# Kernel tuning notes

Measured on AMD Instinct MI355X. Metric: run time of the kernel, lower is better.

## Reference

```python
import jax, jax.numpy as jnp
import numpy as np

N, E, IN_DIM, OUT_DIM, H = 4096, 131072, 1024, 512, 4


def setup_inputs() -> dict:
    key = jax.random.key(0)
    k1, k2, k3, k4 = jax.random.split(key, 4)
    x = jax.random.normal(k1, (N, IN_DIM), dtype=jnp.float32)
    edge_index = jax.random.randint(k2, (2, E), 0, N, dtype=jnp.int64)
    # learned params, scaled like torch Linear init (~1/sqrt(fan_in))
    W = jax.random.normal(k3, (H, IN_DIM, OUT_DIM), dtype=jnp.float32) * 0.02
    a = jax.random.normal(k4, (H, 2 * OUT_DIM), dtype=jnp.float32) * 0.02
    return {"x": x, "edge_index": edge_index, "W": W, "a": a}


def reference(x, edge_index, W, a):
    row, col = edge_index[0], edge_index[1]
    n = x.shape[0]
    h = jnp.einsum('ni,hio->hno', x, W)                    # [H, N, out]
    # per-edge attention logits: a . [h[row] || h[col]]
    a_src, a_dst = a[:, :OUT_DIM], a[:, OUT_DIM:]
    e = (jnp.einsum('heo,ho->he', h[:, row], a_src)
         + jnp.einsum('heo,ho->he', h[:, col], a_dst))      # [H, E]
    e = jnp.where(e > 0, e, 0.2 * e)                        # LeakyReLU(0.2)
    # dense NxN attention matrix exactly as the original (zeros at non-edges
    # DO participate in the row softmax, matching the torch code)
    att = jnp.zeros((H, n, n), dtype=h.dtype).at[:, row, col].set(e)
    att = jax.nn.softmax(att, axis=-1)
    h_prime = jnp.einsum('hnm,hmo->hno', att, h)            # [H, N, out]
    return jnp.transpose(h_prime, (1, 0, 2)).reshape(n, H * OUT_DIM)
```

## Files before the change

### kernel.cpp

```cpp
#include <hip/hip_runtime.h>
#include <stdint.h>

#define NN 4096
#define EE 131072
#define IND 1024
#define OUTD 512
#define NH 4
#define NBKT 8
#define BKT_SHIFT 9

typedef __bf16 bf16x8 __attribute__((ext_vector_type(8)));
typedef float f32x4 __attribute__((ext_vector_type(4)));
typedef float f32x2 __attribute__((ext_vector_type(2)));

__device__ __forceinline__ unsigned short f2bf(float f) {
  unsigned u = __float_as_uint(f);
  u += 0x7FFFu + ((u >> 16) & 1u);
  return (unsigned short)(u >> 16);
}

__global__ void prep_kernel(const float* __restrict__ x, unsigned short* __restrict__ xb,
                            const float* __restrict__ W, unsigned short* __restrict__ Wt) {
  __shared__ float tile[32][33];
  const int bid = blockIdx.x, t = threadIdx.x;
  if (bid < 4096) {
    int i = bid * 256 + t;
    float4 v = ((const float4*)x)[i];
    ushort4 o;
    o.x = f2bf(v.x); o.y = f2bf(v.y); o.z = f2bf(v.z); o.w = f2bf(v.w);
    ((ushort4*)xb)[i] = o;
  } else {
    int b2 = bid - 4096;
    int i0 = (b2 & 31) * 32, o0 = ((b2 >> 5) & 15) * 32, h = b2 >> 9;
    int tx = t & 31, ty = t >> 5;
#pragma unroll
    for (int r = 0; r < 32; r += 8)
      tile[ty + r][tx] = W[((size_t)(h * IND + i0 + ty + r)) * OUTD + o0 + tx];
    __syncthreads();
#pragma unroll
    for (int r = 0; r < 32; r += 8)
      Wt[((size_t)(h * OUTD + o0 + ty + r)) * IND + i0 + tx] = f2bf(tile[tx][ty + r]);
  }
}

__device__ __forceinline__ void gload16(const unsigned short* g, unsigned short* l) {
  __builtin_amdgcn_global_load_lds((const __attribute__((address_space(1))) void*)g,
                                   (__attribute__((address_space(3))) void*)l, 16, 0, 0);
}

__global__ __launch_bounds__(256, 2) void gemm_kernel(
    const unsigned short* __restrict__ X, const unsigned short* __restrict__ Wt,
    const float* __restrict__ Av, unsigned char* __restrict__ Hb8,
    float* __restrict__ s4_src, float* __restrict__ s4_dst, float* __restrict__ Scol) {
  __shared__ __align__(16) unsigned short As[2][4096];
  __shared__ __align__(16) unsigned short Bs[2][4096];
  const int t = threadIdx.x, w = t >> 6, lane = t & 63;
  const int B = blockIdx.x;
  const int L = ((B & 7) << 6) | (B >> 3);
  const int bx = L & 3, hh = (L >> 2) & 3, by = L >> 4;

  const unsigned short* Ab0 = X + (size_t)(by * 128) * IND;
  const unsigned short* Bb0 = Wt + (size_t)(hh * OUTD + bx * 128) * IND;

  const int seg0 = w * 64 + lane, seg1 = (4 + w) * 64 + lane;
  const int r0 = seg0 >> 2, c0 = (seg0 & 3) ^ (r0 & 3);
  const int r1 = seg1 >> 2, c1 = (seg1 & 3) ^ (r1 & 3);

  const int wr = w >> 1, wc = w & 1, g = lane >> 4, rlo = lane & 15;
  int aoff[4], boff[4];
#pragma unroll
  for (int i = 0; i < 4; i++) {
    int ra = wr * 64 + i * 16 + rlo;
    aoff[i] = ra * 64 + ((g ^ (ra & 3)) << 4);
    int rb = wc * 64 + i * 16 + rlo;
    boff[i] = rb * 64 + ((g ^ (rb & 3)) << 4);
  }

  f32x4 zero = {0.f, 0.f, 0.f, 0.f};
  f32x4 acc[4][4];
#pragma unroll
  for (int i = 0; i < 4; i++)
#pragma unroll
    for (int j = 0; j < 4; j++) acc[i][j] = zero;

#define STAGE(buf, kt)                                                   \
  do {                                                                   \
    const unsigned short* ga = Ab0 + (kt) * 32;                          \
    const unsigned short* gb = Bb0 + (kt) * 32;                          \
    gload16(ga + r0 * IND + c0 * 8, &As[buf][w * 512]);                  \
    gload16(ga + r1 * IND + c1 * 8, &As[buf][(4 + w) * 512]);            \
    gload16(gb + r0 * IND + c0 * 8, &Bs[buf][w * 512]);                  \
    gload16(gb + r1 * IND + c1 * 8, &Bs[buf][(4 + w) * 512]);            \
  } while (0)

  STAGE(0, 0);
  __syncthreads();
  int cur = 0;
  for (int kt = 0; kt < 32; ++kt) {
    if (kt != 31) STAGE(cur ^ 1, kt + 1);
    const char* Abuf = (const char*)As[cur];
    const char* Bbuf = (const char*)Bs[cur];
    bf16x8 av[4], bv[4];
#pragma unroll
    for (int i = 0; i < 4; i++) {
      av[i] = *(const bf16x8*)(Abuf + aoff[i]);
      bv[i] = *(const bf16x8*)(Bbuf + boff[i]);
    }
#pragma unroll
    for (int i = 0; i < 4; i++)
#pragma unroll
      for (int j = 0; j < 4; j++)
        acc[i][j] = __builtin_amdgcn_mfma_f32_16x16x32_bf16(av[i], bv[j], acc[i][j], 0, 0, 0);
    __syncthreads();
    cur ^= 1;
  }
#undef STAGE

#pragma unroll
  for (int i = 0; i < 4; i++)
#pragma unroll
    for (int j = 0; j < 4; j++) {
      int mm0 = by * 128 + wr * 64 + i * 16 + g * 4;
      int nn = bx * 128 + wc * 64 + j * 16 + rlo;
#pragma unroll
      for (int q = 0; q < 4; q++) {
        int p = __builtin_amdgcn_cvt_pk_fp8_f32(acc[i][j][q], acc[i][j][q], 0, false);
        Hb8[((size_t)(mm0 + q) * NH + hh) * OUTD + nn] = (unsigned char)p;
      }
    }

  float as_[4], ad_[4];
#pragma unroll
  for (int j = 0; j < 4; j++) {
    int nn = bx * 128 + wc * 64 + j * 16 + rlo;
    as_[j] = Av[hh * 2 * OUTD + nn];
    ad_[j] = Av[hh * 2 * OUTD + OUTD + nn];
  }
#pragma unroll
  for (int i = 0; i < 4; i++)
#pragma unroll
    for (int q = 0; q < 4; q++) {
      float vs = 0.f, vd = 0.f;
#pragma unroll
      for (int j = 0; j < 4; j++) {
        float tv = acc[i][j][q];
        vs += tv * as_[j];
        vd += tv * ad_[j];
      }
#pragma unroll
      for (int m = 1; m < 16; m <<= 1) {
        vs += __shfl_xor(vs, m);
        vd += __shfl_xor(vd, m);
      }
      if (rlo == 0) {
        int r = by * 128 + wr * 64 + i * 16 + g * 4 + q;
        atomicAdd(&s4_src[r * NH + hh], vs);
        atomicAdd(&s4_dst[r * NH + hh], vd);
      }
    }

#pragma unroll
  for (int j = 0; j < 4; j++) {
    float cv = 0.f;
#pragma unroll
    for (int i = 0; i < 4; i++)
#pragma unroll
      for (int q = 0; q < 4; q++) cv += acc[i][j][q];
    cv += __shfl_xor(cv, 16);
    cv += __shfl_xor(cv, 32);
    if (g == 0) {
      int nn = bx * 128 + wc * 64 + j * 16 + rlo;
      atomicAdd(&Scol[hh * OUTD + nn], cv);
    }
  }
}

__global__ void edge_a_kernel(const int* __restrict__ ei, unsigned* __restrict__ bitmap,
                              int* __restrict__ counts2, unsigned char* __restrict__ flags) {
  int e = blockIdx.x * 256 + threadIdx.x;
  int row = ei[e], col = ei[EE + e];
  unsigned key = ((unsigned)row << 12) | (unsigned)col;
  unsigned bit = 1u << (key & 31);
  unsigned old = atomicOr(&bitmap[key >> 5], bit);
  if (old & bit) { flags[e] = 1; return; }
  flags[e] = 0;
  atomicAdd(&counts2[row * NBKT + (col >> BKT_SHIFT)], 1);
}

__global__ __launch_bounds__(1024) void scan_kernel(const int* __restrict__ c2,
                                                    int* __restrict__ off2,
                                                    int* __restrict__ cur2) {
  __shared__ int wtot[16];
  const int t = threadIdx.x, w = t >> 6, lane = t & 63;
  int loc[32];
  const int4* src = (const int4*)c2 + t * 8;
#pragma unroll
  for (int k = 0; k < 8; k++) {
    int4 v = src[k];
    loc[4 * k] = v.x; loc[4 * k + 1] = v.y; loc[4 * k + 2] = v.z; loc[4 * k + 3] = v.w;
  }
  int s = 0;
#pragma unroll
  for (int k = 0; k < 32; k++) s += loc[k];
  int inc = s;
#pragma unroll
  for (int d = 1; d < 64; d <<= 1) {
    int u = __shfl_up(inc, d);
    if (lane >= d) inc += u;
  }
  if (lane == 63) wtot[w] = inc;
  __syncthreads();
  int wpre = 0;
  for (int k = 0; k < 16; k++)
    if (k < w) wpre += wtot[k];
  int o = wpre + inc - s;
  if (t == 1023) off2[NN * NBKT] = o + s;
  int4* od = (int4*)off2 + t * 8;
  int4* cd = (int4*)cur2 + t * 8;
#pragma unroll
  for (int k = 0; k < 8; k++) {
    int4 ov;
    ov.x = o; o += loc[4 * k];
    ov.y = o; o += loc[4 * k + 1];
    ov.z = o; o += loc[4 * k + 2];
    ov.w = o; o += loc[4 * k + 3];
    od[k] = ov;
    cd[k] = ov;
  }
}

__global__ void edge_b_kernel(const int* __restrict__ ei, const unsigned char* __restrict__ flags,
                              const float* __restrict__ s4_src, const float* __restrict__ s4_dst,
                              int* __restrict__ cursor2, int* __restrict__ csr_col,
                              float* __restrict__ csr_g4) {
  int e = blockIdx.x * 256 + threadIdx.x;
  if (flags[e]) return;
  int row = ei[e], col = ei[EE + e];
  int pos = atomicAdd(&cursor2[row * NBKT + (col >> BKT_SHIFT)], 1);
  csr_col[pos] = col;
  float4 ss = *(const float4*)(s4_src + row * NH);
  float4 sd = *(const float4*)(s4_dst + col * NH);
  float4 gv;
  float e0 = ss.x + sd.x; e0 = e0 > 0.f ? e0 : 0.2f * e0; gv.x = expf(e0) - 1.0f;
  float e1 = ss.y + sd.y; e1 = e1 > 0.f ? e1 : 0.2f * e1; gv.y = expf(e1) - 1.0f;
  float e2 = ss.z + sd.z; e2 = e2 > 0.f ? e2 : 0.2f * e2; gv.z = expf(e2) - 1.0f;
  float e3 = ss.w + sd.w; e3 = e3 > 0.f ? e3 : 0.2f * e3; gv.w = expf(e3) - 1.0f;
  *(float4*)(csr_g4 + (size_t)pos * NH) = gv;
}

__global__ __launch_bounds__(256) void finalize_kernel(
    const unsigned char* __restrict__ Hb8,
    const float* __restrict__ S, const int* __restrict__ offsets2,
    const int* __restrict__ csr_col, const float* __restrict__ csr_g4,
    float* __restrict__ out) {
  __shared__ int cols_s[64];
  __shared__ float g_s[4][64];
  const int i = blockIdx.x, t = threadIdx.x;
  const int w = t >> 6, lane = t & 63;

  float acc[8];
  {
    const float4* Sv = (const float4*)(S + w * OUTD + lane * 8);
    float4 s0 = Sv[0], s1 = Sv[1];
    acc[0] = s0.x; acc[1] = s0.y; acc[2] = s0.z; acc[3] = s0.w;
    acc[4] = s1.x; acc[5] = s1.y; acc[6] = s1.z; acc[7] = s1.w;
  }
  float gsum = 0.f;

  const int start = offsets2[i * NBKT];
  const int cnt = offsets2[(i + 1) * NBKT] - start;
  for (int base = 0; base < cnt; base += 64) {
    int nload = min(64, cnt - base);
    __syncthreads();
    if (w == 0) cols_s[lane] = (lane < nload) ? csr_col[start + base + lane] : 0;
    {
      int el = t >> 2;
      float gvv = (el < nload) ? csr_g4[(size_t)(start + base) * NH + t] : 0.f;
      g_s[t & 3][el] = gvv;
    }
    __syncthreads();
#pragma unroll 4
    for (int k = 0; k < nload; k++) {
      int cc = cols_s[k];
      float gg = g_s[w][k];
      gsum += gg;
      uint2 u = *(const uint2*)(Hb8 + ((size_t)(cc * NH + w)) * OUTD + lane * 8);
      f32x2 p0 = __builtin_amdgcn_cvt_pk_f32_fp8(u.x, false);
      f32x2 p1 = __builtin_amdgcn_cvt_pk_f32_fp8(u.x, true);
      f32x2 p2 = __builtin_amdgcn_cvt_pk_f32_fp8(u.y, false);
      f32x2 p3 = __builtin_amdgcn_cvt_pk_f32_fp8(u.y, true);
      acc[0] += gg * p0[0];
      acc[1] += gg * p0[1];
      acc[2] += gg * p1[0];
      acc[3] += gg * p1[1];
      acc[4] += gg * p2[0];
      acc[5] += gg * p2[1];
      acc[6] += gg * p3[0];
      acc[7] += gg * p3[1];
    }
  }

  float inv = 1.0f / ((float)NN + gsum);
  float4 o0, o1;
  o0.x = acc[0] * inv; o0.y = acc[1] * inv; o0.z = acc[2] * inv; o0.w = acc[3] * inv;
  o1.x = acc[4] * inv; o1.y = acc[5] * inv; o1.z = acc[6] * inv; o1.w = acc[7] * inv;
  float* ob = out + (size_t)i * (NH * OUTD) + w * OUTD + lane * 8;
  ((float4*)ob)[0] = o0;
  ((float4*)ob)[1] = o1;
}

extern "C" void kernel_launch(void* const* d_in, const int* in_sizes, int n_in,
                              void* d_out, int out_size, void* d_ws, size_t ws_size,
                              hipStream_t stream) {
  const float* x = (const float*)d_in[0];
  const int* ei = (const int*)d_in[1];
  const float* W = (const float*)d_in[2];
  const float* a = (const float*)d_in[3];
  float* out = (float*)d_out;

  char* ws = (char*)d_ws;
  unsigned short* xb = (unsigned short*)(ws);
  unsigned short* wt = (unsigned short*)(ws + (8ull << 20));
  unsigned char* Hb8 = (unsigned char*)(ws + (12ull << 20));
  char* zreg = ws + (20ull << 20);
  float* s4_src = (float*)(zreg);
  float* s4_dst = (float*)(zreg + 65536);
  float* Scol = (float*)(zreg + 2 * 65536);
  int* counts2 = (int*)(zreg + 2 * 65536 + 8192);
  unsigned* bitmap = (unsigned*)(zreg + 2 * 65536 + 8192 + 131072);
  const size_t ZBYTES = 2 * 65536 + 8192 + 131072 + ((size_t)NN * NN / 8);
  unsigned char* flags = (unsigned char*)(ws + (23ull << 20));
  int* offsets2 = (int*)(ws + (23ull << 20) + 262144);
  int* cursor2 = (int*)(ws + (23ull << 20) + 2 * 262144);
  int* csr_col = (int*)(ws + (24ull << 20));
  float* csr_g4 = (float*)(ws + (25ull << 20));

  hipMemsetAsync(zreg, 0, ZBYTES, stream);

  prep_kernel<<<4096 + 2048, 256, 0, stream>>>(x, xb, W, wt);
  gemm_kernel<<<512, 256, 0, stream>>>(xb, wt, a, Hb8, s4_src, s4_dst, Scol);
  edge_a_kernel<<<EE / 256, 256, 0, stream>>>(ei, bitmap, counts2, flags);
  scan_kernel<<<1, 1024, 0, stream>>>(counts2, offsets2, cursor2);
  edge_b_kernel<<<EE / 256, 256, 0, stream>>>(ei, flags, s4_src, s4_dst, cursor2, csr_col,
                                              csr_g4);
  finalize_kernel<<<NN, 256, 0, stream>>>(Hb8, Scol, offsets2, csr_col, csr_g4, out);
}
```

Measured before the change: 192.7 us.

## Fuse edge dedup into prep, scan into GEMM, compute attention weights in finalize

Merges the edge dedup/count pass into the prep kernel launch and runs the prefix scan as one extra block of the GEMM launch, cutting two kernel launches and their serialization gaps. Per-edge attention weights are no longer written to a CSR array in edge_b; finalize recomputes them from the per-node source/destination scores, trading extra gathers and exp work for less global traffic. The GEMM also drops its block-index remap, changes the LDS swizzle pattern and raises launch_bounds occupancy to 4 blocks per CU, which may affect L2 reuse and register pressure.

```diff
diff --git a/kernel.cpp b/kernel.cpp
--- a/kernel.cpp
+++ b/kernel.cpp
@@ -19,8 +19,10 @@
   return (unsigned short)(u >> 16);
 }
 
-__global__ void prep_kernel(const float* __restrict__ x, unsigned short* __restrict__ xb,
-                            const float* __restrict__ W, unsigned short* __restrict__ Wt) {
+__global__ void prep_edge_kernel(const float* __restrict__ x, unsigned short* __restrict__ xb,
+                                 const float* __restrict__ W, unsigned short* __restrict__ Wt,
+                                 const int* __restrict__ ei, unsigned* __restrict__ bitmap,
+                                 int* __restrict__ counts2, unsigned char* __restrict__ flags) {
   __shared__ float tile[32][33];
   const int bid = blockIdx.x, t = threadIdx.x;
   if (bid < 4096) {
@@ -29,7 +31,7 @@
     ushort4 o;
     o.x = f2bf(v.x); o.y = f2bf(v.y); o.z = f2bf(v.z); o.w = f2bf(v.w);
     ((ushort4*)xb)[i] = o;
-  } else {
+  } else if (bid < 6144) {
     int b2 = bid - 4096;
     int i0 = (b2 & 31) * 32, o0 = ((b2 >> 5) & 15) * 32, h = b2 >> 9;
     int tx = t & 31, ty = t >> 5;
@@ -40,6 +42,15 @@
 #pragma unroll
     for (int r = 0; r < 32; r += 8)
       Wt[((size_t)(h * OUTD + o0 + ty + r)) * IND + i0 + tx] = f2bf(tile[tx][ty + r]);
+  } else {
+    int e = (bid - 6144) * 256 + t;
+    int row = ei[e], col = ei[EE + e];
+    unsigned key = ((unsigned)row << 12) | (unsigned)col;
+    unsigned bit = 1u << (key & 31);
+    unsigned old = atomicOr(&bitmap[key >> 5], bit);
+    if (old & bit) { flags[e] = 1; return; }
+    flags[e] = 0;
+    atomicAdd(&counts2[row * NBKT + (col >> BKT_SHIFT)], 1);
   }
 }
 
@@ -48,32 +59,70 @@
                                    (__attribute__((address_space(3))) void*)l, 16, 0, 0);
 }
 
-__global__ __launch_bounds__(256, 2) void gemm_kernel(
+__device__ void scan_block_256(const int* __restrict__ c2, int* __restrict__ off2,
+                               int* __restrict__ cur2) {
+  __shared__ int wtot[4];
+  const int t = threadIdx.x, w = t >> 6, lane = t & 63;
+  const int4* src = (const int4*)c2 + t * 32;
+  int s = 0;
+  for (int k = 0; k < 32; k++) { int4 v = src[k]; s += v.x + v.y + v.z + v.w; }
+  int inc = s;
+#pragma unroll
+  for (int d = 1; d < 64; d <<= 1) {
+    int u = __shfl_up(inc, d);
+    if (lane >= d) inc += u;
+  }
+  if (lane == 63) wtot[w] = inc;
+  __syncthreads();
+  int wpre = 0;
+#pragma unroll
+  for (int k = 0; k < 4; k++)
+    if (k < w) wpre += wtot[k];
+  int o = wpre + inc - s;
+  if (t == 255) off2[NN * NBKT] = o + s;
+  int4* od = (int4*)off2 + t * 32;
+  int4* cd = (int4*)cur2 + t * 32;
+  for (int k = 0; k < 32; k++) {
+    int4 v = src[k];
+    int4 ov;
+    ov.x = o; o += v.x;
+    ov.y = o; o += v.y;
+    ov.z = o; o += v.z;
+    ov.w = o; o += v.w;
+    od[k] = ov;
+    cd[k] = ov;
+  }
+}
+
+__global__ __launch_bounds__(256, 4) void gemm_scan_kernel(
     const unsigned short* __restrict__ X, const unsigned short* __restrict__ Wt,
     const float* __restrict__ Av, unsigned char* __restrict__ Hb8,
-    float* __restrict__ s4_src, float* __restrict__ s4_dst, float* __restrict__ Scol) {
+    float* __restrict__ s4_src, float* __restrict__ s4_dst, float* __restrict__ Scol,
+    const int* __restrict__ c2, int* __restrict__ off2, int* __restrict__ cur2) {
+  if (blockIdx.x == 512) {
+    scan_block_256(c2, off2, cur2);
+    return;
+  }
   __shared__ __align__(16) unsigned short As[2][4096];
   __shared__ __align__(16) unsigned short Bs[2][4096];
   const int t = threadIdx.x, w = t >> 6, lane = t & 63;
-  const int B = blockIdx.x;
-  const int L = ((B & 7) << 6) | (B >> 3);
-  const int bx = L & 3, hh = (L >> 2) & 3, by = L >> 4;
+  const int bx = blockIdx.x & 3, hh = (blockIdx.x >> 2) & 3, by = blockIdx.x >> 4;
 
   const unsigned short* Ab0 = X + (size_t)(by * 128) * IND;
   const unsigned short* Bb0 = Wt + (size_t)(hh * OUTD + bx * 128) * IND;
 
-  const int seg0 = w * 64 + lane, seg1 = (4 + w) * 64 + lane;
-  const int r0 = seg0 >> 2, c0 = (seg0 & 3) ^ (r0 & 3);
-  const int r1 = seg1 >> 2, c1 = (seg1 & 3) ^ (r1 & 3);
+  const int seg0 = w * 128 + lane, seg1 = w * 128 + 64 + lane;
+  const int sr0 = seg0 >> 2, sc0 = (seg0 & 3) ^ ((sr0 >> 1) & 3);
+  const int sr1 = seg1 >> 2, sc1 = (seg1 & 3) ^ ((sr1 >> 1) & 3);
 
   const int wr = w >> 1, wc = w & 1, g = lane >> 4, rlo = lane & 15;
   int aoff[4], boff[4];
 #pragma unroll
   for (int i = 0; i < 4; i++) {
     int ra = wr * 64 + i * 16 + rlo;
-    aoff[i] = ra * 64 + ((g ^ (ra & 3)) << 4);
+    aoff[i] = ra * 64 + ((g ^ ((ra >> 1) & 3)) << 4);
     int rb = wc * 64 + i * 16 + rlo;
-    boff[i] = rb * 64 + ((g ^ (rb & 3)) << 4);
+    boff[i] = rb * 64 + ((g ^ ((rb >> 1) & 3)) << 4);
   }
 
   f32x4 zero = {0.f, 0.f, 0.f, 0.f};
@@ -83,14 +132,14 @@
 #pragma unroll
     for (int j = 0; j < 4; j++) acc[i][j] = zero;
 
-#define STAGE(buf, kt)                                                   \
-  do {                                                                   \
-    const unsigned short* ga = Ab0 + (kt) * 32;                          \
-    const unsigned short* gb = Bb0 + (kt) * 32;                          \
-    gload16(ga + r0 * IND + c0 * 8, &As[buf][w * 512]);                  \
-    gload16(ga + r1 * IND + c1 * 8, &As[buf][(4 + w) * 512]);            \
-    gload16(gb + r0 * IND + c0 * 8, &Bs[buf][w * 512]);                  \
-    gload16(gb + r1 * IND + c1 * 8, &Bs[buf][(4 + w) * 512]);            \
+#define STAGE(buf, kt)                                               \
+  do {                                                               \
+    const unsigned short* ga = Ab0 + (kt) * 32;                      \
+    const unsigned short* gb = Bb0 + (kt) * 32;                      \
+    gload16(ga + sr0 * IND + sc0 * 8, &As[buf][w * 1024]);           \
+    gload16(ga + sr1 * IND + sc1 * 8, &As[buf][w * 1024 + 512]);     \
+    gload16(gb + sr0 * IND + sc0 * 8, &Bs[buf][w * 1024]);           \
+    gload16(gb + sr1 * IND + sc1 * 8, &Bs[buf][w * 1024 + 512]);     \
   } while (0)
 
   STAGE(0, 0);
@@ -175,89 +224,26 @@
   }
 }
 
-__global__ void edge_a_kernel(const int* __restrict__ ei, unsigned* __restrict__ bitmap,
-                              int* __restrict__ counts2, unsigned char* __restrict__ flags) {
-  int e = blockIdx.x * 256 + threadIdx.x;
-  int row = ei[e], col = ei[EE + e];
-  unsigned key = ((unsigned)row << 12) | (unsigned)col;
-  unsigned bit = 1u << (key & 31);
-  unsigned old = atomicOr(&bitmap[key >> 5], bit);
-  if (old & bit) { flags[e] = 1; return; }
-  flags[e] = 0;
-  atomicAdd(&counts2[row * NBKT + (col >> BKT_SHIFT)], 1);
-}
-
-__global__ __launch_bounds__(1024) void scan_kernel(const int* __restrict__ c2,
-                                                    int* __restrict__ off2,
-                                                    int* __restrict__ cur2) {
-  __shared__ int wtot[16];
-  const int t = threadIdx.x, w = t >> 6, lane = t & 63;
-  int loc[32];
-  const int4* src = (const int4*)c2 + t * 8;
-#pragma unroll
-  for (int k = 0; k < 8; k++) {
-    int4 v = src[k];
-    loc[4 * k] = v.x; loc[4 * k + 1] = v.y; loc[4 * k + 2] = v.z; loc[4 * k + 3] = v.w;
-  }
-  int s = 0;
-#pragma unroll
-  for (int k = 0; k < 32; k++) s += loc[k];
-  int inc = s;
-#pragma unroll
-  for (int d = 1; d < 64; d <<= 1) {
-    int u = __shfl_up(inc, d);
-    if (lane >= d) inc += u;
-  }
-  if (lane == 63) wtot[w] = inc;
-  __syncthreads();
-  int wpre = 0;
-  for (int k = 0; k < 16; k++)
-    if (k < w) wpre += wtot[k];
-  int o = wpre + inc - s;
-  if (t == 1023) off2[NN * NBKT] = o + s;
-  int4* od = (int4*)off2 + t * 8;
-  int4* cd = (int4*)cur2 + t * 8;
-#pragma unroll
-  for (int k = 0; k < 8; k++) {
-    int4 ov;
-    ov.x = o; o += loc[4 * k];
-    ov.y = o; o += loc[4 * k + 1];
-    ov.z = o; o += loc[4 * k + 2];
-    ov.w = o; o += loc[4 * k + 3];
-    od[k] = ov;
-    cd[k] = ov;
-  }
-}
-
 __global__ void edge_b_kernel(const int* __restrict__ ei, const unsigned char* __restrict__ flags,
-                              const float* __restrict__ s4_src, const float* __restrict__ s4_dst,
-                              int* __restrict__ cursor2, int* __restrict__ csr_col,
-                              float* __restrict__ csr_g4) {
+                              int* __restrict__ cursor2, int* __restrict__ csr_col) {
   int e = blockIdx.x * 256 + threadIdx.x;
   if (flags[e]) return;
   int row = ei[e], col = ei[EE + e];
   int pos = atomicAdd(&cursor2[row * NBKT + (col >> BKT_SHIFT)], 1);
   csr_col[pos] = col;
-  float4 ss = *(const float4*)(s4_src + row * NH);
-  float4 sd = *(const float4*)(s4_dst + col * NH);
-  float4 gv;
-  float e0 = ss.x + sd.x; e0 = e0 > 0.f ? e0 : 0.2f * e0; gv.x = expf(e0) - 1.0f;
-  float e1 = ss.y + sd.y; e1 = e1 > 0.f ? e1 : 0.2f * e1; gv.y = expf(e1) - 1.0f;
-  float e2 = ss.z + sd.z; e2 = e2 > 0.f ? e2 : 0.2f * e2; gv.z = expf(e2) - 1.0f;
-  float e3 = ss.w + sd.w; e3 = e3 > 0.f ? e3 : 0.2f * e3; gv.w = expf(e3) - 1.0f;
-  *(float4*)(csr_g4 + (size_t)pos * NH) = gv;
 }
 
 __global__ __launch_bounds__(256) void finalize_kernel(
     const unsigned char* __restrict__ Hb8,
-    const float* __restrict__ S, const int* __restrict__ offsets2,
-    const int* __restrict__ csr_col, const float* __restrict__ csr_g4,
-    float* __restrict__ out) {
+    const float* __restrict__ S, const float* __restrict__ s4_src,
+    const float* __restrict__ s4_dst, const int* __restrict__ offsets2,
+    const int* __restrict__ csr_col, float* __restrict__ out) {
   __shared__ int cols_s[64];
   __shared__ float g_s[4][64];
   const int i = blockIdx.x, t = threadIdx.x;
   const int w = t >> 6, lane = t & 63;
 
+  const float ssrc = s4_src[i * NH + w];
   float acc[8];
   {
     const float4* Sv = (const float4*)(S + w * OUTD + lane * 8);
@@ -273,12 +259,16 @@
     int nload = min(64, cnt - base);
     __syncthreads();
     if (w == 0) cols_s[lane] = (lane < nload) ? csr_col[start + base + lane] : 0;
+    __syncthreads();
     {
-      int el = t >> 2;
-      float gvv = (el < nload) ? csr_g4[(size_t)(start + base) * NH + t] : 0.f;
-      g_s[t & 3][el] = gvv;
-    }
-    __syncthreads();
+      float gg = 0.f;
+      if (lane < nload) {
+        float e0 = ssrc + s4_dst[cols_s[lane] * NH + w];
+        e0 = e0 > 0.f ? e0 : 0.2f * e0;
+        gg = expf(e0) - 1.0f;
+      }
+      g_s[w][lane] = gg;
+    }
 #pragma unroll 4
     for (int k = 0; k < nload; k++) {
       int cc = cols_s[k];
@@ -333,15 +323,13 @@
   int* offsets2 = (int*)(ws + (23ull << 20) + 262144);
   int* cursor2 = (int*)(ws + (23ull << 20) + 2 * 262144);
   int* csr_col = (int*)(ws + (24ull << 20));
-  float* csr_g4 = (float*)(ws + (25ull << 20));
 
   hipMemsetAsync(zreg, 0, ZBYTES, stream);
 
-  prep_kernel<<<4096 + 2048, 256, 0, stream>>>(x, xb, W, wt);
-  gemm_kernel<<<512, 256, 0, stream>>>(xb, wt, a, Hb8, s4_src, s4_dst, Scol);
-  edge_a_kernel<<<EE / 256, 256, 0, stream>>>(ei, bitmap, counts2, flags);
-  scan_kernel<<<1, 1024, 0, stream>>>(counts2, offsets2, cursor2);
-  edge_b_kernel<<<EE / 256, 256, 0, stream>>>(ei, flags, s4_src, s4_dst, cursor2, csr_col,
-                                              csr_g4);
-  finalize_kernel<<<NN, 256, 0, stream>>>(Hb8, Scol, offsets2, csr_col, csr_g4, out);
-}
+  prep_edge_kernel<<<4096 + 2048 + 512, 256, 0, stream>>>(x, xb, W, wt, ei, bitmap, counts2,
+                                                          flags);
+  gemm_scan_kernel<<<513, 256, 0, stream>>>(xb, wt, a, Hb8, s4_src, s4_dst, Scol, counts2,
+                                            offsets2, cursor2);
+  edge_b_kernel<<<EE / 256, 256, 0, stream>>>(ei, flags, cursor2, csr_col);
+  finalize_kernel<<<NN, 256, 0, stream>>>(Hb8, Scol, s4_src, s4_dst, offsets2, csr_col, out);
+}
```

After: 182.5 us. -5.3%, faster.
